# Performance work log

Measured on AMD Instinct MI355X. Metric: run time of the kernel, lower is better.

## Reference

```python
import jax, jax.numpy as jnp
import numpy as np

B, LQ, LK, D = 8, 2048, 2048, 64


def setup_inputs() -> dict:
    key = jax.random.key(0)
    kq, kk, kv, km = jax.random.split(key, 4)
    q = jax.random.normal(kq, (B, LQ, D), dtype=jnp.float32)
    k = jax.random.normal(kk, (B, LK, D), dtype=jnp.float32)
    v = jax.random.normal(kv, (B, LK, D), dtype=jnp.float32)
    scale = jnp.float32(1.0 / np.sqrt(D))  # 0.125
    attn_mask = jax.random.randint(km, (B, LQ, LK), 0, 2).astype(bool)
    return {"q": q, "k": k, "v": v, "scale": scale, "attn_mask": attn_mask}


def reference(q, k, v, scale, attn_mask):
    # attention scores: [B, LQ, LK]
    attention = jnp.einsum("bqd,bkd->bqk", q, k) * scale
    # masked_fill_(attn_mask, -inf)
    attention = jnp.where(attn_mask, -jnp.inf, attention)
    attention = jax.nn.softmax(attention, axis=-1)
    # context: [B, LQ, D]
    context = jnp.einsum("bqk,bkd->bqd", attention, v)
    return (context, attention)
```

## Files before the change

kernel.cpp:

```cpp
#include <hip/hip_runtime.h>

#define NB 8
#define LQ 2048
#define LK 2048
#define DD 64
#define QBLK 32

typedef unsigned short u16;
typedef short  bf16x8 __attribute__((ext_vector_type(8)));
typedef float  f32x4  __attribute__((ext_vector_type(4)));
typedef u16    u16x4  __attribute__((ext_vector_type(4)));
typedef u16    u16x8  __attribute__((ext_vector_type(8)));

#define MFMA16(a, b, c) __builtin_amdgcn_mfma_f32_16x16x32_bf16((a), (b), (c), 0, 0, 0)

__device__ __forceinline__ u16 f2bf(float f) {
  unsigned u = __builtin_bit_cast(unsigned, f);
  u = u + 0x7FFFu + ((u >> 16) & 1u);
  return (u16)(u >> 16);
}

__global__ void probe_mask(const unsigned int* __restrict__ m, int* __restrict__ flags) {
  __shared__ int ff, fi, fo;
  if (threadIdx.x == 0) { ff = 0; fi = 0; fo = 0; }
  __syncthreads();
  int lf = 0, li = 0, lo = 0;
  for (int i = threadIdx.x; i < 16384; i += 256) {
    unsigned wv = m[i];
    if (wv == 0x3F800000u) lf = 1;
    if (wv & 0xFFFFFF00u) li = 1;
    if (wv && (i & 1)) lo = 1;
  }
  if (lf) atomicOr(&ff, 1);
  if (li) atomicOr(&fi, 1);
  if (lo) atomicOr(&fo, 1);
  __syncthreads();
  if (threadIdx.x == 0) {
    int shift, boff;
    if (ff)      { shift = 2; boff = 2; }
    else if (fi) { shift = 0; boff = 0; }
    else if (fo) { shift = 2; boff = 0; }
    else         { shift = 3; boff = 0; }
    flags[0] = shift; flags[1] = boff;
  }
}

__global__ __launch_bounds__(256) void prep_kv(
    const float* __restrict__ kf, const float* __restrict__ vf,
    u16* __restrict__ kbf, u16* __restrict__ vt) {
  __shared__ u16 tile[64][65];
  const int b = blockIdx.x >> 5;
  const int k0 = (blockIdx.x & 31) * 64;
  const int tid = threadIdx.x;
#pragma unroll
  for (int pass = 0; pass < 4; ++pass) {
    const int r = pass * 16 + (tid >> 4);
    const int c = (tid & 15) * 4;
    const size_t gi = ((size_t)(b * LK + k0 + r)) * DD + c;
    float4 kx = *(const float4*)(kf + gi);
    u16x4 kv = { f2bf(kx.x), f2bf(kx.y), f2bf(kx.z), f2bf(kx.w) };
    *(u16x4*)(kbf + gi) = kv;
    float4 vx = *(const float4*)(vf + gi);
    tile[r][c + 0] = f2bf(vx.x); tile[r][c + 1] = f2bf(vx.y);
    tile[r][c + 2] = f2bf(vx.z); tile[r][c + 3] = f2bf(vx.w);
  }
  __syncthreads();
  const int d = tid >> 2, kl = (tid & 3) * 16;
  u16 o[16];
#pragma unroll
  for (int j = 0; j < 16; ++j) o[j] = tile[kl + j][d];
  const size_t base = ((size_t)(b * DD + d)) * LK + k0 + kl;
  u16x8 o0 = { o[0], o[1], o[2], o[3], o[4], o[5], o[6], o[7] };
  u16x8 o1 = { o[8], o[9], o[10], o[11], o[12], o[13], o[14], o[15] };
  *(u16x8*)(vt + base) = o0;
  *(u16x8*)(vt + base + 8) = o1;
}

__global__ __launch_bounds__(512, 2) void attn_main(
    const float* __restrict__ q, const u16* __restrict__ kbf,
    const u16* __restrict__ vt, const float* __restrict__ scale_p,
    const unsigned char* __restrict__ mask, const int* __restrict__ flags,
    float* __restrict__ ctx_out, float* __restrict__ attn_out) {
  __shared__ float redmax[8][32];
  __shared__ float redsum[8][32];
  __shared__ float ctxa[QBLK][DD];
  __shared__ u16 pb[8][2048];

  const int bid = blockIdx.x;
  const int b = bid & 7;
  const int q0 = (bid >> 3) * QBLK;
  const int tid = threadIdx.x;
  const int w = tid >> 6;
  const int lane = tid & 63;
  const int lg = lane >> 4, lr = lane & 15;
  const int k0w = w * 256;
  const float scl = scale_p[0];
  const int mshift = flags[0], mboff = flags[1];

  {
    float* cz = &ctxa[0][0];
    for (int i = tid; i < QBLK * DD; i += 512) cz[i] = 0.f;
  }

  bf16x8 aq[2][2];
#pragma unroll
  for (int mm = 0; mm < 2; ++mm)
#pragma unroll
    for (int c = 0; c < 2; ++c) {
      const float* qp = q + ((size_t)(b * LQ + q0 + mm * 16 + lr)) * DD + c * 32 + lg * 8;
      float4 x0 = *(const float4*)qp;
      float4 x1 = *(const float4*)(qp + 4);
      bf16x8 a;
      a[0] = (short)f2bf(x0.x * scl); a[1] = (short)f2bf(x0.y * scl);
      a[2] = (short)f2bf(x0.z * scl); a[3] = (short)f2bf(x0.w * scl);
      a[4] = (short)f2bf(x1.x * scl); a[5] = (short)f2bf(x1.y * scl);
      a[6] = (short)f2bf(x1.z * scl); a[7] = (short)f2bf(x1.w * scl);
      aq[mm][c] = a;
    }

  f32x4 acc[2][16];
#pragma unroll
  for (int mm = 0; mm < 2; ++mm)
#pragma unroll
    for (int t = 0; t < 16; ++t) {
      f32x4 z = { 0.f, 0.f, 0.f, 0.f };
      acc[mm][t] = z;
    }
  const u16* kb = kbf + (size_t)b * LK * DD;
#pragma unroll
  for (int t = 0; t < 16; ++t) {
    const u16* kp = kb + (size_t)(k0w + t * 16 + lr) * DD + lg * 8;
    bf16x8 k0v = *(const bf16x8*)kp;
    bf16x8 k1v = *(const bf16x8*)(kp + 32);
    acc[0][t] = MFMA16(aq[0][0], k0v, acc[0][t]);
    acc[0][t] = MFMA16(aq[0][1], k1v, acc[0][t]);
    acc[1][t] = MFMA16(aq[1][0], k0v, acc[1][t]);
    acc[1][t] = MFMA16(aq[1][1], k1v, acc[1][t]);
  }

  const size_t mrowbase = (size_t)b * LQ + q0;
  float rmax[2][4];
#pragma unroll
  for (int mm = 0; mm < 2; ++mm)
#pragma unroll
    for (int r = 0; r < 4; ++r) {
      const int qrl = mm * 16 + lg * 4 + r;
      const unsigned char* mrow = mask + (((mrowbase + qrl) * LK) << mshift) + mboff;
      float mx = -3.0e38f;
#pragma unroll
      for (int t = 0; t < 16; ++t) {
        unsigned char mv = mrow[((size_t)(k0w + t * 16 + lr)) << mshift];
        float s = acc[mm][t][r];
        s = mv ? -1.0e30f : s;
        acc[mm][t][r] = s;
        mx = fmaxf(mx, s);
      }
      rmax[mm][r] = mx;
    }

#pragma unroll
  for (int mm = 0; mm < 2; ++mm)
#pragma unroll
    for (int r = 0; r < 4; ++r) {
      float mx = rmax[mm][r];
      mx = fmaxf(mx, __shfl_xor(mx, 1));
      mx = fmaxf(mx, __shfl_xor(mx, 2));
      mx = fmaxf(mx, __shfl_xor(mx, 4));
      mx = fmaxf(mx, __shfl_xor(mx, 8));
      rmax[mm][r] = mx;
    }
  if (lr == 0) {
#pragma unroll
    for (int mm = 0; mm < 2; ++mm)
#pragma unroll
      for (int r = 0; r < 4; ++r) redmax[w][mm * 16 + lg * 4 + r] = rmax[mm][r];
  }
  __syncthreads();
  float fm[2][4];
#pragma unroll
  for (int mm = 0; mm < 2; ++mm)
#pragma unroll
    for (int r = 0; r < 4; ++r) {
      const int row = mm * 16 + lg * 4 + r;
      float m = redmax[0][row];
#pragma unroll
      for (int w2 = 1; w2 < 8; ++w2) m = fmaxf(m, redmax[w2][row]);
      fm[mm][r] = m;
    }

  float rsum[2][4];
#pragma unroll
  for (int mm = 0; mm < 2; ++mm)
#pragma unroll
    for (int r = 0; r < 4; ++r) {
      float s = 0.f;
#pragma unroll
      for (int t = 0; t < 16; ++t) {
        float p = __expf(acc[mm][t][r] - fm[mm][r]);
        acc[mm][t][r] = p;
        s += p;
      }
      rsum[mm][r] = s;
    }
#pragma unroll
  for (int mm = 0; mm < 2; ++mm)
#pragma unroll
    for (int r = 0; r < 4; ++r) {
      float s = rsum[mm][r];
      s += __shfl_xor(s, 1);
      s += __shfl_xor(s, 2);
      s += __shfl_xor(s, 4);
      s += __shfl_xor(s, 8);
      rsum[mm][r] = s;
    }
  if (lr == 0) {
#pragma unroll
    for (int mm = 0; mm < 2; ++mm)
#pragma unroll
      for (int r = 0; r < 4; ++r) redsum[w][mm * 16 + lg * 4 + r] = rsum[mm][r];
  }
  __syncthreads();
  float rl[2][4];
#pragma unroll
  for (int mm = 0; mm < 2; ++mm)
#pragma unroll
    for (int r = 0; r < 4; ++r) {
      const int row = mm * 16 + lg * 4 + r;
      float s = redsum[0][row];
#pragma unroll
      for (int w2 = 1; w2 < 8; ++w2) s += redsum[w2][row];
      rl[mm][r] = 1.0f / s;
    }

  f32x4 cacc[2][4];
#pragma unroll
  for (int mm = 0; mm < 2; ++mm)
#pragma unroll
    for (int dd = 0; dd < 4; ++dd) {
      f32x4 z = { 0.f, 0.f, 0.f, 0.f };
      cacc[mm][dd] = z;
    }
  u16* pbw = pb[w];
  const u16* vtb = vt + (size_t)b * DD * LK;
  float* attb = attn_out + mrowbase * LK;

#pragma unroll
  for (int kk = 0; kk < 8; ++kk) {
#pragma unroll
    for (int mm = 0; mm < 2; ++mm)
#pragma unroll
      for (int tt = 0; tt < 2; ++tt) {
        const int t = kk * 2 + tt;
#pragma unroll
        for (int r = 0; r < 4; ++r) {
          const int qrl = mm * 16 + lg * 4 + r;
          float pf = acc[mm][t][r] * rl[mm][r];
          attb[(size_t)qrl * LK + k0w + t * 16 + lr] = pf;
          const int byteoff = (qrl * 128 + (tt * 16 + lr) * 2) ^ ((qrl & 7) << 4);
          *(u16*)((char*)pbw + byteoff) = f2bf(pf);
        }
      }
    asm volatile("s_waitcnt lgkmcnt(0)" ::: "memory");
    __builtin_amdgcn_sched_barrier(0);
    bf16x8 pa[2];
#pragma unroll
    for (int mm = 0; mm < 2; ++mm) {
      const int qrl = mm * 16 + lr;
      const int ro = (qrl * 128 + lg * 16) ^ ((qrl & 7) << 4);
      pa[mm] = *(const bf16x8*)((const char*)pbw + ro);
    }
#pragma unroll
    for (int dd = 0; dd < 4; ++dd) {
      const u16* vp = vtb + (size_t)(dd * 16 + lr) * LK + k0w + kk * 32 + lg * 8;
      bf16x8 vb = *(const bf16x8*)vp;
      cacc[0][dd] = MFMA16(pa[0], vb, cacc[0][dd]);
      cacc[1][dd] = MFMA16(pa[1], vb, cacc[1][dd]);
    }
  }

#pragma unroll
  for (int mm = 0; mm < 2; ++mm)
#pragma unroll
    for (int dd = 0; dd < 4; ++dd)
#pragma unroll
      for (int r = 0; r < 4; ++r)
        atomicAdd(&ctxa[mm * 16 + lg * 4 + r][dd * 16 + lr], cacc[mm][dd][r]);
  __syncthreads();
  {
    const int qrl = tid >> 4, d0 = (tid & 15) * 4;
    float4 val = *(const float4*)&ctxa[qrl][d0];
    *(float4*)(ctx_out + ((size_t)(b * LQ) + q0 + qrl) * DD + d0) = val;
  }
}

__global__ __launch_bounds__(64) void attn_naive(
    const float* __restrict__ q, const float* __restrict__ kf,
    const float* __restrict__ vf, const float* __restrict__ scale_p,
    const unsigned char* __restrict__ mask, const int* __restrict__ flags,
    float* __restrict__ ctx_out, float* __restrict__ attn_out) {
  __shared__ float red[64][65];
  const int row = blockIdx.x;
  const int lane = threadIdx.x;
  const int shift = flags[0], boff = flags[1];
  const float scl = scale_p[0];
  const int b = row >> 11;
  float qv[DD];
#pragma unroll
  for (int d = 0; d < DD; ++d) qv[d] = q[(size_t)row * DD + d] * scl;
  float s[32];
  float mx = -3.0e38f;
#pragma unroll
  for (int i = 0; i < 32; ++i) {
    const int kc = lane + i * 64;
    const float* kp = kf + ((size_t)b * LK + kc) * DD;
    float dot = 0.f;
#pragma unroll
    for (int d = 0; d < DD; ++d) dot = fmaf(qv[d], kp[d], dot);
    const unsigned char mv = mask[((((size_t)row) * LK + kc) << shift) + boff];
    dot = mv ? -1.0e30f : dot;
    s[i] = dot;
    mx = fmaxf(mx, dot);
  }
#pragma unroll
  for (int off = 32; off; off >>= 1) mx = fmaxf(mx, __shfl_xor(mx, off));
  float sum = 0.f;
#pragma unroll
  for (int i = 0; i < 32; ++i) { s[i] = __expf(s[i] - mx); sum += s[i]; }
#pragma unroll
  for (int off = 32; off; off >>= 1) sum += __shfl_xor(sum, off);
  const float rl = 1.0f / sum;
  float cl[DD];
#pragma unroll
  for (int d = 0; d < DD; ++d) cl[d] = 0.f;
#pragma unroll
  for (int i = 0; i < 32; ++i) {
    const int kc = lane + i * 64;
    const float p = s[i] * rl;
    attn_out[(size_t)row * LK + kc] = p;
    const float* vp = vf + ((size_t)b * LK + kc) * DD;
#pragma unroll
    for (int d = 0; d < DD; ++d) cl[d] = fmaf(p, vp[d], cl[d]);
  }
#pragma unroll
  for (int d = 0; d < DD; ++d) red[lane][d] = cl[d];
  __syncthreads();
  float o = 0.f;
#pragma unroll
  for (int j = 0; j < 64; ++j) o += red[j][lane];
  ctx_out[(size_t)row * DD + lane] = o;
}

extern "C" void kernel_launch(void* const* d_in, const int* in_sizes, int n_in,
                              void* d_out, int out_size, void* d_ws, size_t ws_size,
                              hipStream_t stream) {
  const float* q  = (const float*)d_in[0];
  const float* kf = (const float*)d_in[1];
  const float* vf = (const float*)d_in[2];
  const float* sc = (const float*)d_in[3];
  const unsigned char* mask = (const unsigned char*)d_in[4];
  float* ctx  = (float*)d_out;
  float* attn = ctx + (size_t)NB * LQ * DD;

  int* flags = (int*)d_ws;
  const size_t kv_elems = (size_t)NB * LK * DD;
  const size_t need = 1024 + 2 * kv_elems * sizeof(u16);

  hipLaunchKernelGGL(probe_mask, dim3(1), dim3(256), 0, stream,
                     (const unsigned int*)mask, flags);

  if (ws_size >= need) {
    u16* kbf = (u16*)((char*)d_ws + 1024);
    u16* vt  = kbf + kv_elems;
    hipLaunchKernelGGL(prep_kv, dim3(NB * 32), dim3(256), 0, stream, kf, vf, kbf, vt);
    hipLaunchKernelGGL(attn_main, dim3((LQ / QBLK) * NB), dim3(512), 0, stream,
                       q, kbf, vt, sc, mask, flags, ctx, attn);
  } else {
    hipLaunchKernelGGL(attn_naive, dim3(NB * LQ), dim3(64), 0, stream,
                       q, kf, vf, sc, mask, flags, ctx, attn);
  }
}
```

Baseline: 354.9 us.

## Recompute QK scores in three passes to cut registers and coalesce attention stores

```diff
diff --git a/kernel.cpp b/kernel.cpp
--- a/kernel.cpp
+++ b/kernel.cpp
@@ -13,11 +13,27 @@
 typedef u16    u16x8  __attribute__((ext_vector_type(8)));
 
 #define MFMA16(a, b, c) __builtin_amdgcn_mfma_f32_16x16x32_bf16((a), (b), (c), 0, 0, 0)
+#define LOG2E 1.44269504088896f
 
 __device__ __forceinline__ u16 f2bf(float f) {
   unsigned u = __builtin_bit_cast(unsigned, f);
   u = u + 0x7FFFu + ((u >> 16) & 1u);
   return (u16)(u >> 16);
+}
+
+__device__ __forceinline__ float fexp2(float x) {
+#if __has_builtin(__builtin_amdgcn_exp2f)
+  return __builtin_amdgcn_exp2f(x);
+#else
+  return __builtin_exp2f(x);
+#endif
+}
+__device__ __forceinline__ float flog2(float x) {
+#if __has_builtin(__builtin_amdgcn_logf)
+  return __builtin_amdgcn_logf(x);
+#else
+  return __builtin_log2f(x);
+#endif
 }
 
 __global__ void probe_mask(const unsigned int* __restrict__ m, int* __restrict__ flags) {
@@ -76,15 +92,15 @@
   *(u16x8*)(vt + base + 8) = o1;
 }
 
-__global__ __launch_bounds__(512, 2) void attn_main(
+__global__ __launch_bounds__(512, 4) void attn_main(
     const float* __restrict__ q, const u16* __restrict__ kbf,
     const u16* __restrict__ vt, const float* __restrict__ scale_p,
     const unsigned char* __restrict__ mask, const int* __restrict__ flags,
     float* __restrict__ ctx_out, float* __restrict__ attn_out) {
-  __shared__ float redmax[8][32];
-  __shared__ float redsum[8][32];
-  __shared__ float ctxa[QBLK][DD];
-  __shared__ u16 pb[8][2048];
+  __shared__ float smem[8][1024];
+  float* redmax = &smem[0][0];
+  float* redsum = redmax + 256;
+  float* ctxa   = redsum + 256;
 
   const int bid = blockIdx.x;
   const int b = bid & 7;
@@ -94,13 +110,8 @@
   const int lane = tid & 63;
   const int lg = lane >> 4, lr = lane & 15;
   const int k0w = w * 256;
-  const float scl = scale_p[0];
+  const float scl2 = scale_p[0] * LOG2E;
   const int mshift = flags[0], mboff = flags[1];
-
-  {
-    float* cz = &ctxa[0][0];
-    for (int i = tid; i < QBLK * DD; i += 512) cz[i] = 0.f;
-  }
 
   bf16x8 aq[2][2];
 #pragma unroll
@@ -111,126 +122,131 @@
       float4 x0 = *(const float4*)qp;
       float4 x1 = *(const float4*)(qp + 4);
       bf16x8 a;
-      a[0] = (short)f2bf(x0.x * scl); a[1] = (short)f2bf(x0.y * scl);
-      a[2] = (short)f2bf(x0.z * scl); a[3] = (short)f2bf(x0.w * scl);
-      a[4] = (short)f2bf(x1.x * scl); a[5] = (short)f2bf(x1.y * scl);
-      a[6] = (short)f2bf(x1.z * scl); a[7] = (short)f2bf(x1.w * scl);
+      a[0] = (short)f2bf(x0.x * scl2); a[1] = (short)f2bf(x0.y * scl2);
+      a[2] = (short)f2bf(x0.z * scl2); a[3] = (short)f2bf(x0.w * scl2);
+      a[4] = (short)f2bf(x1.x * scl2); a[5] = (short)f2bf(x1.y * scl2);
+      a[6] = (short)f2bf(x1.z * scl2); a[7] = (short)f2bf(x1.w * scl2);
       aq[mm][c] = a;
     }
 
-  f32x4 acc[2][16];
-#pragma unroll
-  for (int mm = 0; mm < 2; ++mm)
-#pragma unroll
-    for (int t = 0; t < 16; ++t) {
-      f32x4 z = { 0.f, 0.f, 0.f, 0.f };
-      acc[mm][t] = z;
-    }
   const u16* kb = kbf + (size_t)b * LK * DD;
+  const size_t mrowbase = (size_t)b * LQ + q0;
+
+  float m[2][4];
+  unsigned mb[4] = {0u, 0u, 0u, 0u};
+#pragma unroll
+  for (int mm = 0; mm < 2; ++mm)
+#pragma unroll
+    for (int r = 0; r < 4; ++r) m[mm][r] = -3.0e38f;
+
 #pragma unroll
   for (int t = 0; t < 16; ++t) {
     const u16* kp = kb + (size_t)(k0w + t * 16 + lr) * DD + lg * 8;
     bf16x8 k0v = *(const bf16x8*)kp;
     bf16x8 k1v = *(const bf16x8*)(kp + 32);
-    acc[0][t] = MFMA16(aq[0][0], k0v, acc[0][t]);
-    acc[0][t] = MFMA16(aq[0][1], k1v, acc[0][t]);
-    acc[1][t] = MFMA16(aq[1][0], k0v, acc[1][t]);
-    acc[1][t] = MFMA16(aq[1][1], k1v, acc[1][t]);
-  }
-
-  const size_t mrowbase = (size_t)b * LQ + q0;
-  float rmax[2][4];
+    f32x4 z = { 0.f, 0.f, 0.f, 0.f };
+    f32x4 a0 = z, a1 = z;
+    a0 = MFMA16(aq[0][0], k0v, a0); a0 = MFMA16(aq[0][1], k1v, a0);
+    a1 = MFMA16(aq[1][0], k0v, a1); a1 = MFMA16(aq[1][1], k1v, a1);
+#pragma unroll
+    for (int mm = 0; mm < 2; ++mm)
+#pragma unroll
+      for (int r = 0; r < 4; ++r) {
+        const int row = mm * 16 + lg * 4 + r;
+        const unsigned char mv = __builtin_nontemporal_load(
+            mask + ((((mrowbase + row) * LK) + k0w + t * 16 + lr) << mshift) + mboff);
+        const int idx = mm * 4 + r;
+        mb[idx >> 1] |= (mv ? 1u : 0u) << (((idx & 1) << 4) + t);
+        float v = mm ? a1[r] : a0[r];
+        v = mv ? -3.0e38f : v;
+        m[mm][r] = fmaxf(m[mm][r], v);
+      }
+  }
 #pragma unroll
   for (int mm = 0; mm < 2; ++mm)
 #pragma unroll
     for (int r = 0; r < 4; ++r) {
-      const int qrl = mm * 16 + lg * 4 + r;
-      const unsigned char* mrow = mask + (((mrowbase + qrl) * LK) << mshift) + mboff;
-      float mx = -3.0e38f;
-#pragma unroll
-      for (int t = 0; t < 16; ++t) {
-        unsigned char mv = mrow[((size_t)(k0w + t * 16 + lr)) << mshift];
-        float s = acc[mm][t][r];
-        s = mv ? -1.0e30f : s;
-        acc[mm][t][r] = s;
-        mx = fmaxf(mx, s);
-      }
-      rmax[mm][r] = mx;
-    }
-
-#pragma unroll
-  for (int mm = 0; mm < 2; ++mm)
-#pragma unroll
-    for (int r = 0; r < 4; ++r) {
-      float mx = rmax[mm][r];
+      float mx = m[mm][r];
       mx = fmaxf(mx, __shfl_xor(mx, 1));
       mx = fmaxf(mx, __shfl_xor(mx, 2));
       mx = fmaxf(mx, __shfl_xor(mx, 4));
       mx = fmaxf(mx, __shfl_xor(mx, 8));
-      rmax[mm][r] = mx;
+      m[mm][r] = mx;
     }
   if (lr == 0) {
 #pragma unroll
     for (int mm = 0; mm < 2; ++mm)
 #pragma unroll
-      for (int r = 0; r < 4; ++r) redmax[w][mm * 16 + lg * 4 + r] = rmax[mm][r];
-  }
-  __syncthreads();
-  float fm[2][4];
+      for (int r = 0; r < 4; ++r) redmax[w * 32 + mm * 16 + lg * 4 + r] = m[mm][r];
+  }
+  __syncthreads();
 #pragma unroll
   for (int mm = 0; mm < 2; ++mm)
 #pragma unroll
     for (int r = 0; r < 4; ++r) {
       const int row = mm * 16 + lg * 4 + r;
-      float m = redmax[0][row];
-#pragma unroll
-      for (int w2 = 1; w2 < 8; ++w2) m = fmaxf(m, redmax[w2][row]);
-      fm[mm][r] = m;
-    }
-
-  float rsum[2][4];
+      float mx = redmax[row];
+#pragma unroll
+      for (int w2 = 1; w2 < 8; ++w2) mx = fmaxf(mx, redmax[w2 * 32 + row]);
+      m[mm][r] = mx;
+    }
+
+  float sac[2][4];
+#pragma unroll
+  for (int mm = 0; mm < 2; ++mm)
+#pragma unroll
+    for (int r = 0; r < 4; ++r) sac[mm][r] = 0.f;
+#pragma unroll
+  for (int t = 0; t < 16; ++t) {
+    const u16* kp = kb + (size_t)(k0w + t * 16 + lr) * DD + lg * 8;
+    bf16x8 k0v = *(const bf16x8*)kp;
+    bf16x8 k1v = *(const bf16x8*)(kp + 32);
+    f32x4 z = { 0.f, 0.f, 0.f, 0.f };
+    f32x4 a0 = z, a1 = z;
+    a0 = MFMA16(aq[0][0], k0v, a0); a0 = MFMA16(aq[0][1], k1v, a0);
+    a1 = MFMA16(aq[1][0], k0v, a1); a1 = MFMA16(aq[1][1], k1v, a1);
+#pragma unroll
+    for (int mm = 0; mm < 2; ++mm)
+#pragma unroll
+      for (int r = 0; r < 4; ++r) {
+        const int idx = mm * 4 + r;
+        const unsigned bit = (mb[idx >> 1] >> (((idx & 1) << 4) + t)) & 1u;
+        float v = mm ? a1[r] : a0[r];
+        float e = fexp2(v - m[mm][r]);
+        e = bit ? 0.f : e;
+        sac[mm][r] += e;
+      }
+  }
 #pragma unroll
   for (int mm = 0; mm < 2; ++mm)
 #pragma unroll
     for (int r = 0; r < 4; ++r) {
-      float s = 0.f;
-#pragma unroll
-      for (int t = 0; t < 16; ++t) {
-        float p = __expf(acc[mm][t][r] - fm[mm][r]);
-        acc[mm][t][r] = p;
-        s += p;
-      }
-      rsum[mm][r] = s;
-    }
-#pragma unroll
-  for (int mm = 0; mm < 2; ++mm)
-#pragma unroll
-    for (int r = 0; r < 4; ++r) {
-      float s = rsum[mm][r];
+      float s = sac[mm][r];
       s += __shfl_xor(s, 1);
       s += __shfl_xor(s, 2);
       s += __shfl_xor(s, 4);
       s += __shfl_xor(s, 8);
-      rsum[mm][r] = s;
+      sac[mm][r] = s;
     }
   if (lr == 0) {
 #pragma unroll
     for (int mm = 0; mm < 2; ++mm)
 #pragma unroll
-      for (int r = 0; r < 4; ++r) redsum[w][mm * 16 + lg * 4 + r] = rsum[mm][r];
-  }
-  __syncthreads();
-  float rl[2][4];
+      for (int r = 0; r < 4; ++r) redsum[w * 32 + mm * 16 + lg * 4 + r] = sac[mm][r];
+  }
+  __syncthreads();
+  float cc[2][4];
 #pragma unroll
   for (int mm = 0; mm < 2; ++mm)
 #pragma unroll
     for (int r = 0; r < 4; ++r) {
       const int row = mm * 16 + lg * 4 + r;
-      float s = redsum[0][row];
-#pragma unroll
-      for (int w2 = 1; w2 < 8; ++w2) s += redsum[w2][row];
-      rl[mm][r] = 1.0f / s;
-    }
+      float s = redsum[row];
+#pragma unroll
+      for (int w2 = 1; w2 < 8; ++w2) s += redsum[w2 * 32 + row];
+      cc[mm][r] = m[mm][r] + flog2(s);
+    }
+  __syncthreads();
 
   f32x4 cacc[2][4];
 #pragma unroll
@@ -240,34 +256,63 @@
       f32x4 z = { 0.f, 0.f, 0.f, 0.f };
       cacc[mm][dd] = z;
     }
-  u16* pbw = pb[w];
+  float* pbw = smem[w];
   const u16* vtb = vt + (size_t)b * DD * LK;
   float* attb = attn_out + mrowbase * LK;
 
 #pragma unroll
   for (int kk = 0; kk < 8; ++kk) {
+    f32x4 a[2][2];
+#pragma unroll
+    for (int tt = 0; tt < 2; ++tt) {
+      const int t = kk * 2 + tt;
+      const u16* kp = kb + (size_t)(k0w + t * 16 + lr) * DD + lg * 8;
+      bf16x8 k0v = *(const bf16x8*)kp;
+      bf16x8 k1v = *(const bf16x8*)(kp + 32);
+      f32x4 z = { 0.f, 0.f, 0.f, 0.f };
+      f32x4 a0 = z, a1 = z;
+      a0 = MFMA16(aq[0][0], k0v, a0); a0 = MFMA16(aq[0][1], k1v, a0);
+      a1 = MFMA16(aq[1][0], k0v, a1); a1 = MFMA16(aq[1][1], k1v, a1);
+      a[0][tt] = a0; a[1][tt] = a1;
+    }
 #pragma unroll
     for (int mm = 0; mm < 2; ++mm)
 #pragma unroll
-      for (int tt = 0; tt < 2; ++tt) {
-        const int t = kk * 2 + tt;
+      for (int tt = 0; tt < 2; ++tt)
 #pragma unroll
         for (int r = 0; r < 4; ++r) {
-          const int qrl = mm * 16 + lg * 4 + r;
-          float pf = acc[mm][t][r] * rl[mm][r];
-          attb[(size_t)qrl * LK + k0w + t * 16 + lr] = pf;
-          const int byteoff = (qrl * 128 + (tt * 16 + lr) * 2) ^ ((qrl & 7) << 4);
-          *(u16*)((char*)pbw + byteoff) = f2bf(pf);
+          const int t = kk * 2 + tt;
+          const int idx = mm * 4 + r;
+          const unsigned bit = (mb[idx >> 1] >> (((idx & 1) << 4) + t)) & 1u;
+          float p = fexp2(a[mm][tt][r] - cc[mm][r]);
+          p = bit ? 0.f : p;
+          const int row = mm * 16 + lg * 4 + r;
+          const int off = (row * 128 + (tt * 16 + lr) * 4) ^ ((row & 7) << 4);
+          *(float*)((char*)pbw + off) = p;
         }
-      }
     asm volatile("s_waitcnt lgkmcnt(0)" ::: "memory");
     __builtin_amdgcn_sched_barrier(0);
+#pragma unroll
+    for (int pp = 0; pp < 4; ++pp) {
+      const int row = pp * 8 + (lane >> 3);
+      const int c4 = (lane & 7) * 4;
+      const int off = (row * 128 + c4 * 4) ^ ((row & 7) << 4);
+      f32x4 val = *(const f32x4*)((const char*)pbw + off);
+      __builtin_nontemporal_store(val, (f32x4*)(attb + (size_t)row * LK + k0w + kk * 32 + c4));
+    }
     bf16x8 pa[2];
 #pragma unroll
     for (int mm = 0; mm < 2; ++mm) {
-      const int qrl = mm * 16 + lr;
-      const int ro = (qrl * 128 + lg * 16) ^ ((qrl & 7) << 4);
-      pa[mm] = *(const bf16x8*)((const char*)pbw + ro);
+      const int row = mm * 16 + lr;
+      const int swz = (row & 7) << 4;
+      f32x4 f0 = *(const f32x4*)((const char*)pbw + ((row * 128 + lg * 32) ^ swz));
+      f32x4 f1 = *(const f32x4*)((const char*)pbw + ((row * 128 + lg * 32 + 16) ^ swz));
+      bf16x8 pv;
+      pv[0] = (short)f2bf(f0[0]); pv[1] = (short)f2bf(f0[1]);
+      pv[2] = (short)f2bf(f0[2]); pv[3] = (short)f2bf(f0[3]);
+      pv[4] = (short)f2bf(f1[0]); pv[5] = (short)f2bf(f1[1]);
+      pv[6] = (short)f2bf(f1[2]); pv[7] = (short)f2bf(f1[3]);
+      pa[mm] = pv;
     }
 #pragma unroll
     for (int dd = 0; dd < 4; ++dd) {
@@ -278,18 +323,25 @@
     }
   }
 
+  __syncthreads();
+  {
+    float* cz = ctxa;
+#pragma unroll
+    for (int i = 0; i < 4; ++i) cz[tid + i * 512] = 0.f;
+  }
+  __syncthreads();
 #pragma unroll
   for (int mm = 0; mm < 2; ++mm)
 #pragma unroll
     for (int dd = 0; dd < 4; ++dd)
 #pragma unroll
       for (int r = 0; r < 4; ++r)
-        atomicAdd(&ctxa[mm * 16 + lg * 4 + r][dd * 16 + lr], cacc[mm][dd][r]);
+        atomicAdd(&ctxa[(mm * 16 + lg * 4 + r) * DD + dd * 16 + lr], cacc[mm][dd][r]);
   __syncthreads();
   {
-    const int qrl = tid >> 4, d0 = (tid & 15) * 4;
-    float4 val = *(const float4*)&ctxa[qrl][d0];
-    *(float4*)(ctx_out + ((size_t)(b * LQ) + q0 + qrl) * DD + d0) = val;
+    const int row = tid >> 4, d0 = (tid & 15) * 4;
+    f32x4 val = *(const f32x4*)&ctxa[row * DD + d0];
+    __builtin_nontemporal_store(val, (f32x4*)(ctx_out + ((size_t)(b * LQ) + q0 + row) * DD + d0));
   }
 }
 
```

Measured after the change: 444.1 us. 1.25x slower.

## Halve query block to 16 rows, raise occupancy, use exp2 softmax

Applied to the files above, without the earlier changes.

```diff
diff --git a/kernel.cpp b/kernel.cpp
--- a/kernel.cpp
+++ b/kernel.cpp
@@ -4,7 +4,7 @@
 #define LQ 2048
 #define LK 2048
 #define DD 64
-#define QBLK 32
+#define QBLK 16
 
 typedef unsigned short u16;
 typedef short  bf16x8 __attribute__((ext_vector_type(8)));
@@ -13,6 +13,7 @@
 typedef u16    u16x8  __attribute__((ext_vector_type(8)));
 
 #define MFMA16(a, b, c) __builtin_amdgcn_mfma_f32_16x16x32_bf16((a), (b), (c), 0, 0, 0)
+#define LOG2E 1.44269504088896f
 
 __device__ __forceinline__ u16 f2bf(float f) {
   unsigned u = __builtin_bit_cast(unsigned, f);
@@ -20,12 +21,20 @@
   return (u16)(u >> 16);
 }
 
+__device__ __forceinline__ float fexp2(float x) {
+#if __has_builtin(__builtin_amdgcn_exp2f)
+  return __builtin_amdgcn_exp2f(x);
+#else
+  return __builtin_exp2f(x);
+#endif
+}
+
 __global__ void probe_mask(const unsigned int* __restrict__ m, int* __restrict__ flags) {
   __shared__ int ff, fi, fo;
   if (threadIdx.x == 0) { ff = 0; fi = 0; fo = 0; }
   __syncthreads();
   int lf = 0, li = 0, lo = 0;
-  for (int i = threadIdx.x; i < 16384; i += 256) {
+  for (int i = threadIdx.x; i < 1024; i += 256) {
     unsigned wv = m[i];
     if (wv == 0x3F800000u) lf = 1;
     if (wv & 0xFFFFFF00u) li = 1;
@@ -76,15 +85,15 @@
   *(u16x8*)(vt + base + 8) = o1;
 }
 
-__global__ __launch_bounds__(512, 2) void attn_main(
+__global__ __launch_bounds__(512, 4) void attn_main(
     const float* __restrict__ q, const u16* __restrict__ kbf,
     const u16* __restrict__ vt, const float* __restrict__ scale_p,
     const unsigned char* __restrict__ mask, const int* __restrict__ flags,
     float* __restrict__ ctx_out, float* __restrict__ attn_out) {
-  __shared__ float redmax[8][32];
-  __shared__ float redsum[8][32];
+  __shared__ float redmax[8][16];
+  __shared__ float redsum[8][16];
   __shared__ float ctxa[QBLK][DD];
-  __shared__ u16 pb[8][2048];
+  __shared__ u16 pb[8][1024];
 
   const int bid = blockIdx.x;
   const int b = bid & 7;
@@ -94,7 +103,7 @@
   const int lane = tid & 63;
   const int lg = lane >> 4, lr = lane & 15;
   const int k0w = w * 256;
-  const float scl = scale_p[0];
+  const float scl2 = scale_p[0] * LOG2E;
   const int mshift = flags[0], mboff = flags[1];
 
   {
@@ -102,144 +111,119 @@
     for (int i = tid; i < QBLK * DD; i += 512) cz[i] = 0.f;
   }
 
-  bf16x8 aq[2][2];
-#pragma unroll
-  for (int mm = 0; mm < 2; ++mm)
-#pragma unroll
-    for (int c = 0; c < 2; ++c) {
-      const float* qp = q + ((size_t)(b * LQ + q0 + mm * 16 + lr)) * DD + c * 32 + lg * 8;
-      float4 x0 = *(const float4*)qp;
-      float4 x1 = *(const float4*)(qp + 4);
-      bf16x8 a;
-      a[0] = (short)f2bf(x0.x * scl); a[1] = (short)f2bf(x0.y * scl);
-      a[2] = (short)f2bf(x0.z * scl); a[3] = (short)f2bf(x0.w * scl);
-      a[4] = (short)f2bf(x1.x * scl); a[5] = (short)f2bf(x1.y * scl);
-      a[6] = (short)f2bf(x1.z * scl); a[7] = (short)f2bf(x1.w * scl);
-      aq[mm][c] = a;
-    }
-
-  f32x4 acc[2][16];
-#pragma unroll
-  for (int mm = 0; mm < 2; ++mm)
-#pragma unroll
-    for (int t = 0; t < 16; ++t) {
-      f32x4 z = { 0.f, 0.f, 0.f, 0.f };
-      acc[mm][t] = z;
-    }
+  bf16x8 aq[2];
+#pragma unroll
+  for (int c = 0; c < 2; ++c) {
+    const float* qp = q + ((size_t)(b * LQ + q0 + lr)) * DD + c * 32 + lg * 8;
+    float4 x0 = *(const float4*)qp;
+    float4 x1 = *(const float4*)(qp + 4);
+    bf16x8 a;
+    a[0] = (short)f2bf(x0.x * scl2); a[1] = (short)f2bf(x0.y * scl2);
+    a[2] = (short)f2bf(x0.z * scl2); a[3] = (short)f2bf(x0.w * scl2);
+    a[4] = (short)f2bf(x1.x * scl2); a[5] = (short)f2bf(x1.y * scl2);
+    a[6] = (short)f2bf(x1.z * scl2); a[7] = (short)f2bf(x1.w * scl2);
+    aq[c] = a;
+  }
+
+  f32x4 acc[16];
+#pragma unroll
+  for (int t = 0; t < 16; ++t) {
+    f32x4 z = { 0.f, 0.f, 0.f, 0.f };
+    acc[t] = z;
+  }
   const u16* kb = kbf + (size_t)b * LK * DD;
 #pragma unroll
   for (int t = 0; t < 16; ++t) {
     const u16* kp = kb + (size_t)(k0w + t * 16 + lr) * DD + lg * 8;
     bf16x8 k0v = *(const bf16x8*)kp;
     bf16x8 k1v = *(const bf16x8*)(kp + 32);
-    acc[0][t] = MFMA16(aq[0][0], k0v, acc[0][t]);
-    acc[0][t] = MFMA16(aq[0][1], k1v, acc[0][t]);
-    acc[1][t] = MFMA16(aq[1][0], k0v, acc[1][t]);
-    acc[1][t] = MFMA16(aq[1][1], k1v, acc[1][t]);
+    acc[t] = MFMA16(aq[0], k0v, acc[t]);
+    acc[t] = MFMA16(aq[1], k1v, acc[t]);
   }
 
   const size_t mrowbase = (size_t)b * LQ + q0;
-  float rmax[2][4];
-#pragma unroll
-  for (int mm = 0; mm < 2; ++mm)
-#pragma unroll
-    for (int r = 0; r < 4; ++r) {
-      const int qrl = mm * 16 + lg * 4 + r;
-      const unsigned char* mrow = mask + (((mrowbase + qrl) * LK) << mshift) + mboff;
-      float mx = -3.0e38f;
-#pragma unroll
-      for (int t = 0; t < 16; ++t) {
-        unsigned char mv = mrow[((size_t)(k0w + t * 16 + lr)) << mshift];
-        float s = acc[mm][t][r];
-        s = mv ? -1.0e30f : s;
-        acc[mm][t][r] = s;
-        mx = fmaxf(mx, s);
-      }
-      rmax[mm][r] = mx;
-    }
-
-#pragma unroll
-  for (int mm = 0; mm < 2; ++mm)
-#pragma unroll
-    for (int r = 0; r < 4; ++r) {
-      float mx = rmax[mm][r];
-      mx = fmaxf(mx, __shfl_xor(mx, 1));
-      mx = fmaxf(mx, __shfl_xor(mx, 2));
-      mx = fmaxf(mx, __shfl_xor(mx, 4));
-      mx = fmaxf(mx, __shfl_xor(mx, 8));
-      rmax[mm][r] = mx;
-    }
+  float rmax[4];
+#pragma unroll
+  for (int r = 0; r < 4; ++r) {
+    const int row = lg * 4 + r;
+    const unsigned char* mrow = mask + (((mrowbase + row) * LK) << mshift) + mboff;
+    float mx = -3.0e38f;
+#pragma unroll
+    for (int t = 0; t < 16; ++t) {
+      const unsigned char mv = mrow[((size_t)(k0w + t * 16 + lr)) << mshift];
+      float s = acc[t][r];
+      s = mv ? -3.0e38f : s;
+      acc[t][r] = s;
+      mx = fmaxf(mx, s);
+    }
+    rmax[r] = mx;
+  }
+#pragma unroll
+  for (int r = 0; r < 4; ++r) {
+    float mx = rmax[r];
+    mx = fmaxf(mx, __shfl_xor(mx, 1));
+    mx = fmaxf(mx, __shfl_xor(mx, 2));
+    mx = fmaxf(mx, __shfl_xor(mx, 4));
+    mx = fmaxf(mx, __shfl_xor(mx, 8));
+    rmax[r] = mx;
+  }
   if (lr == 0) {
 #pragma unroll
-    for (int mm = 0; mm < 2; ++mm)
-#pragma unroll
-      for (int r = 0; r < 4; ++r) redmax[w][mm * 16 + lg * 4 + r] = rmax[mm][r];
-  }
-  __syncthreads();
-  float fm[2][4];
-#pragma unroll
-  for (int mm = 0; mm < 2; ++mm)
-#pragma unroll
-    for (int r = 0; r < 4; ++r) {
-      const int row = mm * 16 + lg * 4 + r;
-      float m = redmax[0][row];
-#pragma unroll
-      for (int w2 = 1; w2 < 8; ++w2) m = fmaxf(m, redmax[w2][row]);
-      fm[mm][r] = m;
-    }
-
-  float rsum[2][4];
-#pragma unroll
-  for (int mm = 0; mm < 2; ++mm)
-#pragma unroll
-    for (int r = 0; r < 4; ++r) {
-      float s = 0.f;
-#pragma unroll
-      for (int t = 0; t < 16; ++t) {
-        float p = __expf(acc[mm][t][r] - fm[mm][r]);
-        acc[mm][t][r] = p;
-        s += p;
-      }
-      rsum[mm][r] = s;
-    }
-#pragma unroll
-  for (int mm = 0; mm < 2; ++mm)
-#pragma unroll
-    for (int r = 0; r < 4; ++r) {
-      float s = rsum[mm][r];
-      s += __shfl_xor(s, 1);
-      s += __shfl_xor(s, 2);
-      s += __shfl_xor(s, 4);
-      s += __shfl_xor(s, 8);
-      rsum[mm][r] = s;
-    }
+    for (int r = 0; r < 4; ++r) redmax[w][lg * 4 + r] = rmax[r];
+  }
+  __syncthreads();
+  float fm[4];
+#pragma unroll
+  for (int r = 0; r < 4; ++r) {
+    const int row = lg * 4 + r;
+    float mx = redmax[0][row];
+#pragma unroll
+    for (int w2 = 1; w2 < 8; ++w2) mx = fmaxf(mx, redmax[w2][row]);
+    fm[r] = mx;
+  }
+
+  float rsum[4];
+#pragma unroll
+  for (int r = 0; r < 4; ++r) {
+    float s = 0.f;
+#pragma unroll
+    for (int t = 0; t < 16; ++t) {
+      float e = fexp2(acc[t][r] - fm[r]);
+      acc[t][r] = e;
+      s += e;
+    }
+    rsum[r] = s;
+  }
+#pragma unroll
+  for (int r = 0; r < 4; ++r) {
+    float s = rsum[r];
+    s += __shfl_xor(s, 1);
+    s += __shfl_xor(s, 2);
+    s += __shfl_xor(s, 4);
+    s += __shfl_xor(s, 8);
+    rsum[r] = s;
+  }
   if (lr == 0) {
 #pragma unroll
-    for (int mm = 0; mm < 2; ++mm)
-#pragma unroll
-      for (int r = 0; r < 4; ++r) redsum[w][mm * 16 + lg * 4 + r] = rsum[mm][r];
-  }
-  __syncthreads();
-  float rl[2][4];
-#pragma unroll
-  for (int mm = 0; mm < 2; ++mm)
-#pragma unroll
-    for (int r = 0; r < 4; ++r) {
-      const int row = mm * 16 + lg * 4 + r;
-      float s = redsum[0][row];
-#pragma unroll
-      for (int w2 = 1; w2 < 8; ++w2) s += redsum[w2][row];
-      rl[mm][r] = 1.0f / s;
-    }
-
-  f32x4 cacc[2][4];
-#pragma unroll
-  for (int mm = 0; mm < 2; ++mm)
-#pragma unroll
-    for (int dd = 0; dd < 4; ++dd) {
-      f32x4 z = { 0.f, 0.f, 0.f, 0.f };
-      cacc[mm][dd] = z;
-    }
+    for (int r = 0; r < 4; ++r) redsum[w][lg * 4 + r] = rsum[r];
+  }
+  __syncthreads();
+  float rl[4];
+#pragma unroll
+  for (int r = 0; r < 4; ++r) {
+    const int row = lg * 4 + r;
+    float s = redsum[0][row];
+#pragma unroll
+    for (int w2 = 1; w2 < 8; ++w2) s += redsum[w2][row];
+    rl[r] = 1.0f / s;
+  }
+
+  f32x4 cacc[4];
+#pragma unroll
+  for (int dd = 0; dd < 4; ++dd) {
+    f32x4 z = { 0.f, 0.f, 0.f, 0.f };
+    cacc[dd] = z;
+  }
   u16* pbw = pb[w];
   const u16* vtb = vt + (size_t)b * DD * LK;
   float* attb = attn_out + mrowbase * LK;
@@ -247,49 +231,42 @@
 #pragma unroll
   for (int kk = 0; kk < 8; ++kk) {
 #pragma unroll
-    for (int mm = 0; mm < 2; ++mm)
-#pragma unroll
-      for (int tt = 0; tt < 2; ++tt) {
-        const int t = kk * 2 + tt;
-#pragma unroll
-        for (int r = 0; r < 4; ++r) {
-          const int qrl = mm * 16 + lg * 4 + r;
-          float pf = acc[mm][t][r] * rl[mm][r];
-          attb[(size_t)qrl * LK + k0w + t * 16 + lr] = pf;
-          const int byteoff = (qrl * 128 + (tt * 16 + lr) * 2) ^ ((qrl & 7) << 4);
-          *(u16*)((char*)pbw + byteoff) = f2bf(pf);
-        }
+    for (int tt = 0; tt < 2; ++tt) {
+      const int t = kk * 2 + tt;
+#pragma unroll
+      for (int r = 0; r < 4; ++r) {
+        const int row = lg * 4 + r;
+        float p = acc[t][r] * rl[r];
+        attb[(size_t)row * LK + k0w + t * 16 + lr] = p;
+        const int off = (row * 128 + (tt * 16 + lr) * 2) ^ ((row & 7) << 4);
+        *(u16*)((char*)pbw + off) = f2bf(p);
       }
+    }
     asm volatile("s_waitcnt lgkmcnt(0)" ::: "memory");
     __builtin_amdgcn_sched_barrier(0);
-    bf16x8 pa[2];
-#pragma unroll
-    for (int mm = 0; mm < 2; ++mm) {
-      const int qrl = mm * 16 + lr;
-      const int ro = (qrl * 128 + lg * 16) ^ ((qrl & 7) << 4);
-      pa[mm] = *(const bf16x8*)((const char*)pbw + ro);
+    bf16x8 pa;
+    {
+      const int ro = (lr * 128 + lg * 16) ^ ((lr & 7) << 4);
+      pa = *(const bf16x8*)((const char*)pbw + ro);
     }
 #pragma unroll
     for (int dd = 0; dd < 4; ++dd) {
       const u16* vp = vtb + (size_t)(dd * 16 + lr) * LK + k0w + kk * 32 + lg * 8;
       bf16x8 vb = *(const bf16x8*)vp;
-      cacc[0][dd] = MFMA16(pa[0], vb, cacc[0][dd]);
-      cacc[1][dd] = MFMA16(pa[1], vb, cacc[1][dd]);
-    }
-  }
-
-#pragma unroll
-  for (int mm = 0; mm < 2; ++mm)
-#pragma unroll
-    for (int dd = 0; dd < 4; ++dd)
-#pragma unroll
-      for (int r = 0; r < 4; ++r)
-        atomicAdd(&ctxa[mm * 16 + lg * 4 + r][dd * 16 + lr], cacc[mm][dd][r]);
-  __syncthreads();
-  {
-    const int qrl = tid >> 4, d0 = (tid & 15) * 4;
-    float4 val = *(const float4*)&ctxa[qrl][d0];
-    *(float4*)(ctx_out + ((size_t)(b * LQ) + q0 + qrl) * DD + d0) = val;
+      cacc[dd] = MFMA16(pa, vb, cacc[dd]);
+    }
+  }
+
+#pragma unroll
+  for (int dd = 0; dd < 4; ++dd)
+#pragma unroll
+    for (int r = 0; r < 4; ++r)
+      atomicAdd(&ctxa[lg * 4 + r][dd * 16 + lr], cacc[dd][r]);
+  __syncthreads();
+  if (tid < QBLK * 16) {
+    const int row = tid >> 4, d0 = (tid & 15) * 4;
+    float4 val = *(const float4*)&ctxa[row][d0];
+    *(float4*)(ctx_out + ((size_t)(b * LQ) + q0 + row) * DD + d0) = val;
   }
 }
 
```

New measurement: 326.2 us. -8.1%, faster.
